# Kernel tuning notes

Measured on AMD Instinct MI355X. Metric: run time of the kernel, lower is better.

The kernel has to match this reference:

```python
import jax, jax.numpy as jnp
import numpy as np


def setup_inputs() -> dict:
    key = jax.random.key(0)
    k1, k2 = jax.random.split(key)
    B, D, T_ENC, T_DEC = 16, 256, 512, 2048
    x = jax.random.normal(k1, (B, D, T_ENC), dtype=jnp.float32)
    path = jax.random.uniform(k2, (B, T_ENC, T_DEC), dtype=jnp.float32)
    return {"x": x, "path": path}


def reference(x, path):
    # Batched matmul: [B, D, T_enc] @ [B, T_enc, T_dec] -> [B, D, T_dec]
    return jnp.einsum('bde,bet->bdt', x, path)
```

## Files before the change

kernel.cpp:

```cpp
#include <hip/hip_runtime.h>
#include <hip/hip_bf16.h>

#define NB 16
#define ND 256
#define NK 512
#define NT 2048

#define BM 128
#define BN 128
#define BK 32
#define RSA 40
#define RSB 36

typedef __attribute__((ext_vector_type(8))) short short8;
typedef __attribute__((ext_vector_type(4))) float f32x4;

union S8U { short8 v; uint2 u[2]; };
union BF2U { __hip_bfloat162 h; unsigned int u; };

__device__ inline unsigned int pack2bf(float a, float b) {
    BF2U c; c.h = __float22bfloat162_rn(make_float2(a, b));
    return c.u;
}

__global__ __launch_bounds__(256, 2)
void bmm_bf16_mfma(const float* __restrict__ x, const float* __restrict__ path,
                   float* __restrict__ out) {
    const int n0 = blockIdx.x * BN;
    const int m0 = blockIdx.y * BM;
    const int b  = blockIdx.z;
    const int t    = threadIdx.x;
    const int lane = t & 63;
    const int wv   = t >> 6;
    const int wr   = (wv >> 1) * 64;
    const int wc   = (wv & 1) * 64;
    const int q    = lane >> 4;
    const int lm   = lane & 15;

    __shared__ unsigned short As[BM * RSA];
    __shared__ unsigned short Bs[BN * RSB];

    const float* xg = x    + ((size_t)b * ND + m0) * NK;
    const float* pg = path + (size_t)b * NK * NT + n0;

    f32x4 acc[4][4];
#pragma unroll
    for (int i = 0; i < 4; ++i)
#pragma unroll
        for (int j = 0; j < 4; ++j)
            acc[i][j] = (f32x4){0.f, 0.f, 0.f, 0.f};

    for (int k0 = 0; k0 < NK; k0 += BK) {
#pragma unroll
        for (int i = 0; i < 4; ++i) {
            int f   = t + i * 256;
            int row = f >> 3;
            int c4  = f & 7;
            float4 v = *reinterpret_cast<const float4*>(xg + (size_t)row * NK + k0 + c4 * 4);
            uint2 p;
            p.x = pack2bf(v.x, v.y);
            p.y = pack2bf(v.z, v.w);
            *reinterpret_cast<uint2*>(&As[row * RSA + c4 * 4]) = p;
        }
#pragma unroll
        for (int i = 0; i < 4; ++i) {
            int p   = wv * 4 + i;
            int kr4 = p >> 1;
            int ng  = p & 1;
            int n   = ng * 64 + lane;
            const float* src = pg + (size_t)(k0 + kr4 * 4) * NT + n;
            float f0 = src[0 * NT];
            float f1 = src[1 * NT];
            float f2 = src[2 * NT];
            float f3 = src[3 * NT];
            uint2 pk;
            pk.x = pack2bf(f0, f1);
            pk.y = pack2bf(f2, f3);
            *reinterpret_cast<uint2*>(&Bs[n * RSB + kr4 * 4]) = pk;
        }
        __syncthreads();

        short8 af[4];
        short8 bfr[4];
#pragma unroll
        for (int mt = 0; mt < 4; ++mt) {
            int row = wr + mt * 16 + lm;
            af[mt] = *reinterpret_cast<const short8*>(&As[row * RSA + q * 8]);
        }
#pragma unroll
        for (int nt = 0; nt < 4; ++nt) {
            int n = wc + nt * 16 + lm;
            S8U s;
            s.u[0] = *reinterpret_cast<const uint2*>(&Bs[n * RSB + q * 8]);
            s.u[1] = *reinterpret_cast<const uint2*>(&Bs[n * RSB + q * 8 + 4]);
            bfr[nt] = s.v;
        }
#pragma unroll
        for (int mt = 0; mt < 4; ++mt)
#pragma unroll
            for (int nt = 0; nt < 4; ++nt)
                acc[mt][nt] = __builtin_amdgcn_mfma_f32_16x16x32_bf16(
                    af[mt], bfr[nt], acc[mt][nt], 0, 0, 0);

        __syncthreads();
    }

    float* og = out + ((size_t)b * ND + m0 + wr) * NT + n0 + wc;
#pragma unroll
    for (int mt = 0; mt < 4; ++mt) {
#pragma unroll
        for (int r = 0; r < 4; ++r) {
            int row = mt * 16 + q * 4 + r;
#pragma unroll
            for (int nt = 0; nt < 4; ++nt) {
                int col = nt * 16 + lm;
                og[(size_t)row * NT + col] = acc[mt][nt][r];
            }
        }
    }
}

extern "C" void kernel_launch(void* const* d_in, const int* in_sizes, int n_in,
                              void* d_out, int out_size, void* d_ws, size_t ws_size,
                              hipStream_t stream) {
    const float* x    = (const float*)d_in[0];
    const float* path = (const float*)d_in[1];
    float* out        = (float*)d_out;
    dim3 grid(NT / BN, ND / BM, NB);
    dim3 block(256);
    bmm_bf16_mfma<<<grid, block, 0, stream>>>(x, path, out);
}
```

Measured before the change: 119.0 us.

## Double-buffer LDS tiles with register prefetch and vectorize output stores

After: 139.8 us. 1.18x slower.

```diff
diff --git a/kernel.cpp b/kernel.cpp
--- a/kernel.cpp
+++ b/kernel.cpp
@@ -9,6 +9,7 @@
 #define BM 128
 #define BN 128
 #define BK 32
+#define NSTEP (NK / BK)
 #define RSA 40
 #define RSB 36
 
@@ -37,11 +38,14 @@
     const int q    = lane >> 4;
     const int lm   = lane & 15;
 
-    __shared__ unsigned short As[BM * RSA];
-    __shared__ unsigned short Bs[BN * RSB];
+    __shared__ unsigned short As[2][BM * RSA];
+    __shared__ unsigned short Bs[2][BN * RSB];
 
     const float* xg = x    + ((size_t)b * ND + m0) * NK;
     const float* pg = path + (size_t)b * NK * NT + n0;
+
+    const int rowA = t >> 3;
+    const int c4   = t & 7;
 
     f32x4 acc[4][4];
 #pragma unroll
@@ -50,74 +54,92 @@
         for (int j = 0; j < 4; ++j)
             acc[i][j] = (f32x4){0.f, 0.f, 0.f, 0.f};
 
-    for (int k0 = 0; k0 < NK; k0 += BK) {
+    float4 pa[4];
+    float  pb[4][4];
+
+    auto load_tile = [&](int k0) {
+#pragma unroll
+        for (int i = 0; i < 4; ++i)
+            pa[i] = *reinterpret_cast<const float4*>(
+                xg + (size_t)(rowA + i * 32) * NK + k0 + c4 * 4);
 #pragma unroll
         for (int i = 0; i < 4; ++i) {
-            int f   = t + i * 256;
-            int row = f >> 3;
-            int c4  = f & 7;
-            float4 v = *reinterpret_cast<const float4*>(xg + (size_t)row * NK + k0 + c4 * 4);
-            uint2 p;
-            p.x = pack2bf(v.x, v.y);
-            p.y = pack2bf(v.z, v.w);
-            *reinterpret_cast<uint2*>(&As[row * RSA + c4 * 4]) = p;
+            const int p   = wv * 4 + i;
+            const int kr4 = p >> 1;
+            const int n   = (p & 1) * 64 + lane;
+            const float* src = pg + (size_t)(k0 + kr4 * 4) * NT + n;
+            pb[i][0] = src[0 * NT];
+            pb[i][1] = src[1 * NT];
+            pb[i][2] = src[2 * NT];
+            pb[i][3] = src[3 * NT];
+        }
+    };
+
+    auto write_tile = [&](int bsel) {
+#pragma unroll
+        for (int i = 0; i < 4; ++i) {
+            uint2 w;
+            w.x = pack2bf(pa[i].x, pa[i].y);
+            w.y = pack2bf(pa[i].z, pa[i].w);
+            *reinterpret_cast<uint2*>(&As[bsel][(rowA + i * 32) * RSA + c4 * 4]) = w;
         }
 #pragma unroll
         for (int i = 0; i < 4; ++i) {
-            int p   = wv * 4 + i;
-            int kr4 = p >> 1;
-            int ng  = p & 1;
-            int n   = ng * 64 + lane;
-            const float* src = pg + (size_t)(k0 + kr4 * 4) * NT + n;
-            float f0 = src[0 * NT];
-            float f1 = src[1 * NT];
-            float f2 = src[2 * NT];
-            float f3 = src[3 * NT];
-            uint2 pk;
-            pk.x = pack2bf(f0, f1);
-            pk.y = pack2bf(f2, f3);
-            *reinterpret_cast<uint2*>(&Bs[n * RSB + kr4 * 4]) = pk;
+            const int p   = wv * 4 + i;
+            const int kr4 = p >> 1;
+            const int n   = (p & 1) * 64 + lane;
+            uint2 w;
+            w.x = pack2bf(pb[i][0], pb[i][1]);
+            w.y = pack2bf(pb[i][2], pb[i][3]);
+            *reinterpret_cast<uint2*>(&Bs[bsel][n * RSB + kr4 * 4]) = w;
         }
-        __syncthreads();
+    };
 
+    auto compute = [&](int bsel) {
         short8 af[4];
-        short8 bfr[4];
+        short8 bfrg[4];
 #pragma unroll
-        for (int mt = 0; mt < 4; ++mt) {
-            int row = wr + mt * 16 + lm;
-            af[mt] = *reinterpret_cast<const short8*>(&As[row * RSA + q * 8]);
-        }
+        for (int mt = 0; mt < 4; ++mt)
+            af[mt] = *reinterpret_cast<const short8*>(
+                &As[bsel][(wr + mt * 16 + lm) * RSA + q * 8]);
 #pragma unroll
         for (int nt = 0; nt < 4; ++nt) {
-            int n = wc + nt * 16 + lm;
             S8U s;
-            s.u[0] = *reinterpret_cast<const uint2*>(&Bs[n * RSB + q * 8]);
-            s.u[1] = *reinterpret_cast<const uint2*>(&Bs[n * RSB + q * 8 + 4]);
-            bfr[nt] = s.v;
+            s.u[0] = *reinterpret_cast<const uint2*>(
+                &Bs[bsel][(wc + nt * 16 + lm) * RSB + q * 8]);
+            s.u[1] = *reinterpret_cast<const uint2*>(
+                &Bs[bsel][(wc + nt * 16 + lm) * RSB + q * 8 + 4]);
+            bfrg[nt] = s.v;
         }
 #pragma unroll
         for (int mt = 0; mt < 4; ++mt)
 #pragma unroll
             for (int nt = 0; nt < 4; ++nt)
                 acc[mt][nt] = __builtin_amdgcn_mfma_f32_16x16x32_bf16(
-                    af[mt], bfr[nt], acc[mt][nt], 0, 0, 0);
+                    bfrg[nt], af[mt], acc[mt][nt], 0, 0, 0);
+    };
 
+    load_tile(0);
+    write_tile(0);
+    __syncthreads();
+
+    int cur = 0;
+    for (int s = 0; s < NSTEP - 1; ++s) {
+        load_tile((s + 1) * BK);
+        compute(cur);
+        write_tile(cur ^ 1);
         __syncthreads();
+        cur ^= 1;
     }
+    compute(cur);
 
     float* og = out + ((size_t)b * ND + m0 + wr) * NT + n0 + wc;
 #pragma unroll
-    for (int mt = 0; mt < 4; ++mt) {
+    for (int mt = 0; mt < 4; ++mt)
 #pragma unroll
-        for (int r = 0; r < 4; ++r) {
-            int row = mt * 16 + q * 4 + r;
-#pragma unroll
-            for (int nt = 0; nt < 4; ++nt) {
-                int col = nt * 16 + lm;
-                og[(size_t)row * NT + col] = acc[mt][nt][r];
-            }
-        }
-    }
+        for (int nt = 0; nt < 4; ++nt)
+            *reinterpret_cast<f32x4*>(
+                &og[(size_t)(mt * 16 + lm) * NT + nt * 16 + q * 4]) = acc[mt][nt];
 }
 
 extern "C" void kernel_launch(void* const* d_in, const int* in_sizes, int n_in,
```

## Double K tile, swizzle block order across XCDs, and vectorize output stores

Applied to the files above, without the earlier changes.

After: 175.1 us. 47.2% more time.

```diff
diff --git a/kernel.cpp b/kernel.cpp
--- a/kernel.cpp
+++ b/kernel.cpp
@@ -8,9 +8,9 @@
 
 #define BM 128
 #define BN 128
-#define BK 32
-#define RSA 40
-#define RSB 36
+#define BK 64
+#define RSA 72
+#define RSB 68
 
 typedef __attribute__((ext_vector_type(8))) short short8;
 typedef __attribute__((ext_vector_type(4))) float f32x4;
@@ -26,9 +26,13 @@
 __global__ __launch_bounds__(256, 2)
 void bmm_bf16_mfma(const float* __restrict__ x, const float* __restrict__ path,
                    float* __restrict__ out) {
-    const int n0 = blockIdx.x * BN;
-    const int m0 = blockIdx.y * BM;
-    const int b  = blockIdx.z;
+    const int id  = blockIdx.x;
+    const int swz = (id & 7) * 64 + (id >> 3);
+    const int b   = swz >> 5;
+    const int rem = swz & 31;
+    const int n0  = (rem >> 1) * BN;
+    const int m0  = (rem & 1)  * BM;
+
     const int t    = threadIdx.x;
     const int lane = t & 63;
     const int wv   = t >> 6;
@@ -52,10 +56,10 @@
 
     for (int k0 = 0; k0 < NK; k0 += BK) {
 #pragma unroll
-        for (int i = 0; i < 4; ++i) {
+        for (int i = 0; i < 8; ++i) {
             int f   = t + i * 256;
-            int row = f >> 3;
-            int c4  = f & 7;
+            int row = f >> 4;
+            int c4  = f & 15;
             float4 v = *reinterpret_cast<const float4*>(xg + (size_t)row * NK + k0 + c4 * 4);
             uint2 p;
             p.x = pack2bf(v.x, v.y);
@@ -63,8 +67,8 @@
             *reinterpret_cast<uint2*>(&As[row * RSA + c4 * 4]) = p;
         }
 #pragma unroll
-        for (int i = 0; i < 4; ++i) {
-            int p   = wv * 4 + i;
+        for (int i = 0; i < 8; ++i) {
+            int p   = wv * 8 + i;
             int kr4 = p >> 1;
             int ng  = p & 1;
             int n   = ng * 64 + lane;
@@ -80,44 +84,42 @@
         }
         __syncthreads();
 
-        short8 af[4];
-        short8 bfr[4];
 #pragma unroll
-        for (int mt = 0; mt < 4; ++mt) {
-            int row = wr + mt * 16 + lm;
-            af[mt] = *reinterpret_cast<const short8*>(&As[row * RSA + q * 8]);
+        for (int ks = 0; ks < 2; ++ks) {
+            short8 af[4];
+            short8 bfr[4];
+#pragma unroll
+            for (int mt = 0; mt < 4; ++mt) {
+                int row = wr + mt * 16 + lm;
+                af[mt] = *reinterpret_cast<const short8*>(
+                    &As[row * RSA + ks * 32 + q * 8]);
+            }
+#pragma unroll
+            for (int nt = 0; nt < 4; ++nt) {
+                int n = wc + nt * 16 + lm;
+                S8U s;
+                s.u[0] = *reinterpret_cast<const uint2*>(&Bs[n * RSB + ks * 32 + q * 8]);
+                s.u[1] = *reinterpret_cast<const uint2*>(&Bs[n * RSB + ks * 32 + q * 8 + 4]);
+                bfr[nt] = s.v;
+            }
+#pragma unroll
+            for (int mt = 0; mt < 4; ++mt)
+#pragma unroll
+                for (int nt = 0; nt < 4; ++nt)
+                    acc[mt][nt] = __builtin_amdgcn_mfma_f32_16x16x32_bf16(
+                        bfr[nt], af[mt], acc[mt][nt], 0, 0, 0);
         }
-#pragma unroll
-        for (int nt = 0; nt < 4; ++nt) {
-            int n = wc + nt * 16 + lm;
-            S8U s;
-            s.u[0] = *reinterpret_cast<const uint2*>(&Bs[n * RSB + q * 8]);
-            s.u[1] = *reinterpret_cast<const uint2*>(&Bs[n * RSB + q * 8 + 4]);
-            bfr[nt] = s.v;
-        }
-#pragma unroll
-        for (int mt = 0; mt < 4; ++mt)
-#pragma unroll
-            for (int nt = 0; nt < 4; ++nt)
-                acc[mt][nt] = __builtin_amdgcn_mfma_f32_16x16x32_bf16(
-                    af[mt], bfr[nt], acc[mt][nt], 0, 0, 0);
 
         __syncthreads();
     }
 
     float* og = out + ((size_t)b * ND + m0 + wr) * NT + n0 + wc;
 #pragma unroll
-    for (int mt = 0; mt < 4; ++mt) {
+    for (int mt = 0; mt < 4; ++mt)
 #pragma unroll
-        for (int r = 0; r < 4; ++r) {
-            int row = mt * 16 + q * 4 + r;
-#pragma unroll
-            for (int nt = 0; nt < 4; ++nt) {
-                int col = nt * 16 + lm;
-                og[(size_t)row * NT + col] = acc[mt][nt][r];
-            }
-        }
-    }
+        for (int nt = 0; nt < 4; ++nt)
+            *reinterpret_cast<f32x4*>(
+                &og[(size_t)(mt * 16 + lm) * NT + nt * 16 + q * 4]) = acc[mt][nt];
 }
 
 extern "C" void kernel_launch(void* const* d_in, const int* in_sizes, int n_in,
@@ -126,7 +128,7 @@
     const float* x    = (const float*)d_in[0];
     const float* path = (const float*)d_in[1];
     float* out        = (float*)d_out;
-    dim3 grid(NT / BN, ND / BM, NB);
+    dim3 grid(512);
     dim3 block(256);
     bmm_bf16_mfma<<<grid, block, 0, stream>>>(x, path, out);
 }
```
